# Performance work log

Measured on AMD Instinct MI355X. Metric: run time of the kernel, lower is better.

Reference implementation:

```python
import jax, jax.numpy as jnp
import numpy as np

N = 50000      # total nodes
E = 800000     # directed edges
G = 512        # graphs in batch
F_IN = 64      # node feature dim
H = 128        # hidden dim
L = 3          # gnn layers
OUT = 12       # tox21 tasks
EPS = 1e-5


def layer_norm(h, gamma, beta):
    mu = jnp.mean(h, axis=-1, keepdims=True)
    var = jnp.mean(jnp.square(h - mu), axis=-1, keepdims=True)
    return (h - mu) * jax.lax.rsqrt(var + EPS) * gamma + beta


def setup_inputs() -> dict:
    key = jax.random.key(0)
    ks = jax.random.split(key, 20)
    x = jax.random.normal(ks[0], (N, F_IN), jnp.float32)
    edge_index = jax.random.randint(ks[1], (2, E), 0, N, dtype=jnp.int64)
    batch_ids = jnp.sort(jax.random.randint(ks[2], (N,), 0, G, dtype=jnp.int64))
    s_in = 1.0 / np.sqrt(F_IN)
    s_h = 1.0 / np.sqrt(H)
    return {
        "x": x,
        "edge_index": edge_index,
        "batch_ids": batch_ids,
        "W_embed": jax.random.normal(ks[3], (F_IN, H), jnp.float32) * s_in,
        "b_embed": jnp.zeros((H,), jnp.float32),
        "g_embed": jnp.ones((H,), jnp.float32),
        "be_embed": jnp.zeros((H,), jnp.float32),
        "W_conv": jax.random.normal(ks[4], (L, H, H), jnp.float32) * s_h,
        "b_conv": jnp.zeros((L, H), jnp.float32),
        "g_ln": jnp.ones((L, H), jnp.float32),
        "b_ln": jnp.zeros((L, H), jnp.float32),
        "W_r1": jax.random.normal(ks[5], (H, H // 2), jnp.float32) * s_h,
        "b_r1": jnp.zeros((H // 2,), jnp.float32),
        "W_r2": jax.random.normal(ks[6], (H // 2, OUT), jnp.float32) * (1.0 / np.sqrt(H // 2)),
        "b_r2": jnp.zeros((OUT,), jnp.float32),
    }


def reference(x, edge_index, batch_ids, W_embed, b_embed, g_embed, be_embed,
              W_conv, b_conv, g_ln, b_ln, W_r1, b_r1, W_r2, b_r2):
    n = x.shape[0]
    # node embedding: Linear -> LayerNorm -> ReLU (dropout = eval identity)
    h = jax.nn.relu(layer_norm(x @ W_embed + b_embed, g_embed, be_embed))

    # GCN normalization with self-loops (PyG GCNConv semantics)
    loop = jnp.arange(n, dtype=edge_index.dtype)
    src = jnp.concatenate([edge_index[0], loop])  # message sources
    dst = jnp.concatenate([edge_index[1], loop])  # message targets
    deg = jax.ops.segment_sum(jnp.ones_like(dst, dtype=h.dtype), dst, num_segments=N)
    dinv = jnp.where(deg > 0, jax.lax.rsqrt(deg), 0.0)
    norm = dinv[src] * dinv[dst]  # [E+N]

    for i in range(L):
        h_prev = h
        m = h @ W_conv[i]                                        # [N,H] linear first
        msg = m[src] * norm[:, None]                             # gather + scale
        agg = jax.ops.segment_sum(msg, dst, num_segments=N)      # scatter-add
        agg = agg + b_conv[i]                                    # bias after aggregation
        h = jax.nn.relu(layer_norm(agg, g_ln[i], b_ln[i])) + h_prev  # norm+relu+residual

    # global mean pooling per graph
    counts = jax.ops.segment_sum(jnp.ones((n,), h.dtype), batch_ids, num_segments=G)
    pooled = jax.ops.segment_sum(h, batch_ids, num_segments=G) / jnp.maximum(counts, 1.0)[:, None]

    # readout MLP
    r = jax.nn.relu(pooled @ W_r1 + b_r1)
    return r @ W_r2 + b_r2
```

## Files before the change

### kernel.cpp

```cpp
#include <hip/hip_runtime.h>

#define HDIM 128
#define FIN 64
#define EPS 1e-5f
#define ECH 2048

typedef unsigned int uint;
typedef unsigned short ushort;
typedef __attribute__((ext_vector_type(8))) short bf16x8;
typedef __attribute__((ext_vector_type(4))) float f32x4;

__device__ __forceinline__ ushort f2bf(float f) {
    uint u = __float_as_uint(f);
    return (ushort)((u + 0x7fffu + ((u >> 16) & 1u)) >> 16);
}
__device__ __forceinline__ float bflo(uint u) { return __uint_as_float(u << 16); }
__device__ __forceinline__ float bfhi(uint u) { return __uint_as_float(u & 0xffff0000u); }

__global__ __launch_bounds__(256) void embed_fused(
    const float* __restrict__ x, const float* __restrict__ W,
    const float* __restrict__ b, const float* __restrict__ g,
    const float* __restrict__ be, ushort* __restrict__ hbf, int nrows,
    const int* __restrict__ dst, int* __restrict__ cnt, int e, int divc,
    const float* __restrict__ Wc, ushort* __restrict__ Wt)
{
    int t = threadIdx.x;
    int gtid = blockIdx.x * 256 + t;
    if (gtid < 3 * HDIM * HDIM) {
        int l = gtid >> 14, rem = gtid & 16383;
        int k = rem >> 7, nn = rem & 127;
        Wt[(l << 14) + nn * HDIM + k] = f2bf(Wc[gtid]);
    }
    int gpart = blockIdx.x & 7;
    int base = (blockIdx.x >> 3) * ECH;
    for (int i = t; i < ECH; i += 256) {
        int idx = base + i;
        if (idx < e) {
            int d = dst[idx];
            if ((int)((uint)d / (uint)divc) == gpart) atomicAdd(&cnt[d], 1);
        }
    }

    int row0 = blockIdx.x * 32;
    if (row0 >= nrows) return;

    __shared__ float Ws[FIN * HDIM];
    __shared__ float xs[32 * FIN];
    const float4* W4 = (const float4*)W;
    float4* Ws4 = (float4*)Ws;
#pragma unroll
    for (int i = 0; i < (FIN * HDIM / 4) / 256; i++) Ws4[t + i * 256] = W4[t + i * 256];
    int nr = nrows - row0; if (nr > 32) nr = 32;
    const float4* x4 = (const float4*)(x + (size_t)row0 * FIN);
    float4* xs4 = (float4*)xs;
    for (int i = t; i < nr * (FIN / 4); i += 256) xs4[i] = x4[i];
    __syncthreads();

    int c = (t & 31) * 4;
    int r0 = (t >> 5) * 4;
    float acc[4][4];
    float4 bv = *(const float4*)(b + c);
#pragma unroll
    for (int i = 0; i < 4; i++) { acc[i][0] = bv.x; acc[i][1] = bv.y; acc[i][2] = bv.z; acc[i][3] = bv.w; }
#pragma unroll 8
    for (int k = 0; k < FIN; k++) {
        float4 wv = *(const float4*)(Ws + k * HDIM + c);
#pragma unroll
        for (int i = 0; i < 4; i++) {
            float xv = xs[(r0 + i) * FIN + k];
            acc[i][0] += xv * wv.x; acc[i][1] += xv * wv.y;
            acc[i][2] += xv * wv.z; acc[i][3] += xv * wv.w;
        }
    }
    float4 gv = *(const float4*)(g + c);
    float4 bev = *(const float4*)(be + c);
#pragma unroll
    for (int i = 0; i < 4; i++) {
        float s1 = acc[i][0] + acc[i][1] + acc[i][2] + acc[i][3];
        float s2 = acc[i][0]*acc[i][0] + acc[i][1]*acc[i][1] + acc[i][2]*acc[i][2] + acc[i][3]*acc[i][3];
#pragma unroll
        for (int m = 16; m; m >>= 1) { s1 += __shfl_xor(s1, m); s2 += __shfl_xor(s2, m); }
        float mu = s1 * (1.0f / HDIM);
        float var = s2 * (1.0f / HDIM) - mu * mu;
        float rstd = rsqrtf(var + EPS);
        int row = row0 + r0 + i;
        if (row < nrows) {
            float ox = fmaxf((acc[i][0] - mu) * rstd * gv.x + bev.x, 0.f);
            float oy = fmaxf((acc[i][1] - mu) * rstd * gv.y + bev.y, 0.f);
            float oz = fmaxf((acc[i][2] - mu) * rstd * gv.z + bev.z, 0.f);
            float ow = fmaxf((acc[i][3] - mu) * rstd * gv.w + bev.w, 0.f);
            uint2 hb;
            hb.x = ((uint)f2bf(oy) << 16) | f2bf(ox);
            hb.y = ((uint)f2bf(ow) << 16) | f2bf(oz);
            *(uint2*)(hbf + (size_t)row * HDIM + c) = hb;
        }
    }
}

__global__ __launch_bounds__(256) void scan_sums(const int* __restrict__ cnt, int* __restrict__ bsum)
{
    __shared__ int s[256];
    int t = threadIdx.x;
    s[t] = cnt[blockIdx.x * 256 + t];
    __syncthreads();
    for (int d = 128; d; d >>= 1) { if (t < d) s[t] += s[t + d]; __syncthreads(); }
    if (t == 0) bsum[blockIdx.x] = s[0];
}

__global__ __launch_bounds__(256) void scan_final(
    const int* __restrict__ cnt, const int* __restrict__ bsum,
    int* __restrict__ rowstart, float* __restrict__ dinv, int nb)
{
    __shared__ int sb[256];
    __shared__ int s[256];
    int t = threadIdx.x;
    int vb = (t < nb) ? bsum[t] : 0;
    sb[t] = vb; __syncthreads();
    for (int d = 1; d < 256; d <<= 1) {
        int xv = (t >= d) ? sb[t - d] : 0;
        __syncthreads();
        sb[t] += xv;
        __syncthreads();
    }
    int blkoff = (blockIdx.x > 0) ? sb[blockIdx.x - 1] : 0;
    int gi = blockIdx.x * 256 + t;
    int c = cnt[gi];
    s[t] = c; __syncthreads();
    for (int d = 1; d < 256; d <<= 1) {
        int xv = (t >= d) ? s[t - d] : 0;
        __syncthreads();
        s[t] += xv;
        __syncthreads();
    }
    rowstart[gi] = blkoff + s[t] - c;
    dinv[gi] = rsqrtf((float)(c + 1));
}

__global__ __launch_bounds__(256) void fill_part(
    const int* __restrict__ src, const int* __restrict__ dst,
    const int* __restrict__ rowstart, int* __restrict__ fill,
    ushort* __restrict__ csr, int e, int divc)
{
    int g = blockIdx.x & 7;
    int base = (blockIdx.x >> 3) * ECH;
    for (int i = threadIdx.x; i < ECH; i += 256) {
        int idx = base + i;
        if (idx < e) {
            int d = dst[idx];
            if ((int)((uint)d / (uint)divc) == g) {
                int s = src[idx];
                int p = rowstart[d] + atomicAdd(&fill[d], 1);
                csr[p] = (ushort)s;
            }
        }
    }
}

__global__ __launch_bounds__(256) void gemm_mfma_kernel(
    const ushort* __restrict__ hbf, const ushort* __restrict__ Wt,
    const float* __restrict__ dinv, ushort* __restrict__ mbf, int nrows)
{
    __shared__ ushort hs[64 * HDIM];
    __shared__ ushort ws[HDIM * HDIM];
    int t = threadIdx.x;
    int wid = t >> 6, lane = t & 63;
    int row0 = blockIdx.x * 64;

#pragma unroll
    for (int it = 0; it < 4; it++) {
        int chunk = t * 4 + it;
        int r = chunk >> 4;
        int offb = (chunk & 15) * 16;
        int gr = row0 + r; if (gr >= nrows) gr = nrows - 1;
        uint4 d = *(const uint4*)(hbf + (size_t)gr * HDIM + (offb >> 1));
        *(uint4*)((char*)hs + r * 256 + (offb ^ ((r & 7) << 4))) = d;
    }
#pragma unroll
    for (int it = 0; it < 8; it++) {
        int chunk = t * 8 + it;
        int r = chunk >> 4;
        int offb = (chunk & 15) * 16;
        uint4 d = *(const uint4*)(Wt + (size_t)r * HDIM + (offb >> 1));
        *(uint4*)((char*)ws + r * 256 + (offb ^ ((r & 7) << 4))) = d;
    }
    __syncthreads();

    f32x4 acc[8];
#pragma unroll
    for (int nt = 0; nt < 8; nt++) acc[nt] = (f32x4){0.f, 0.f, 0.f, 0.f};

    int arow = wid * 16 + (lane & 15);
    int kgrp = (lane >> 4) * 16;
#pragma unroll
    for (int ks = 0; ks < 4; ks++) {
        int kb = ks * 64 + kgrp;
        bf16x8 afrag = *(const bf16x8*)((const char*)hs + arow * 256 + (kb ^ ((arow & 7) << 4)));
#pragma unroll
        for (int nt = 0; nt < 8; nt++) {
            int nrow = nt * 16 + (lane & 15);
            bf16x8 bfrag = *(const bf16x8*)((const char*)ws + nrow * 256 + (kb ^ ((nrow & 7) << 4)));
            acc[nt] = __builtin_amdgcn_mfma_f32_16x16x32_bf16(afrag, bfrag, acc[nt], 0, 0, 0);
        }
    }

    int rbase = row0 + wid * 16 + ((lane >> 4) << 2);
#pragma unroll
    for (int q = 0; q < 4; q++) {
        int grow = rbase + q;
        if (grow < nrows) {
            float dv = dinv[grow];
            ushort* orow = mbf + (size_t)grow * HDIM + (lane & 15);
#pragma unroll
            for (int nt = 0; nt < 8; nt++)
                orow[nt * 16] = f2bf(acc[nt][q] * dv);
        }
    }
}

__global__ __launch_bounds__(256) void agg_kernel(
    const ushort* __restrict__ mbf, const ushort* __restrict__ csr, const int* __restrict__ rowstart,
    const float* __restrict__ dinv, const float* __restrict__ bc,
    const float* __restrict__ gl, const float* __restrict__ bl,
    const ushort* __restrict__ hbf_in, ushort* __restrict__ hbf_out, int n)
{
    int wave = threadIdx.x >> 6, lane = threadIdx.x & 63;
    int v = blockIdx.x * 4 + wave;
    if (v >= n) return;
    const uint* m1 = (const uint*)mbf;
    uint aa = m1[(size_t)v * 64 + lane];
    float ax = bflo(aa), ay = bfhi(aa);
    int s0 = rowstart[v];
    int deg = rowstart[v + 1] - s0;
    for (int base = 0; base < deg; base += 64) {
        int idx = base + lane;
        int my = (idx < deg) ? (int)csr[s0 + idx] : 0;
        int cc = deg - base; if (cc > 64) cc = 64;
        int i = 0;
        for (; i + 4 <= cc; i += 4) {
            int u0 = __shfl(my, i);
            int u1 = __shfl(my, i + 1);
            int u2 = __shfl(my, i + 2);
            int u3 = __shfl(my, i + 3);
            uint w0 = m1[(size_t)u0 * 64 + lane];
            uint w1 = m1[(size_t)u1 * 64 + lane];
            uint w2 = m1[(size_t)u2 * 64 + lane];
            uint w3 = m1[(size_t)u3 * 64 + lane];
            ax += bflo(w0); ay += bfhi(w0);
            ax += bflo(w1); ay += bfhi(w1);
            ax += bflo(w2); ay += bfhi(w2);
            ax += bflo(w3); ay += bfhi(w3);
        }
        for (; i < cc; ++i) {
            int u0 = __shfl(my, i);
            uint w0 = m1[(size_t)u0 * 64 + lane];
            ax += bflo(w0); ay += bfhi(w0);
        }
    }
    float dvv = dinv[v];
    float2 bcv = ((const float2*)bc)[lane];
    float vx = ax * dvv + bcv.x;
    float vy = ay * dvv + bcv.y;
    float s1v = vx + vy, s2v = vx * vx + vy * vy;
#pragma unroll
    for (int m = 32; m; m >>= 1) { s1v += __shfl_xor(s1v, m); s2v += __shfl_xor(s2v, m); }
    float mu = s1v * (1.f / 128.f);
    float var = s2v * (1.f / 128.f) - mu * mu;
    float rstd = rsqrtf(var + EPS);
    float2 gv = ((const float2*)gl)[lane];
    float2 blv = ((const float2*)bl)[lane];
    uint hp = ((const uint*)hbf_in)[(size_t)v * 64 + lane];
    float ox = fmaxf((vx - mu) * rstd * gv.x + blv.x, 0.f) + bflo(hp);
    float oy = fmaxf((vy - mu) * rstd * gv.y + blv.y, 0.f) + bfhi(hp);
    ((uint*)hbf_out)[(size_t)v * 64 + lane] = ((uint)f2bf(oy) << 16) | f2bf(ox);
}

__global__ __launch_bounds__(256) void pool_readout(
    const ushort* __restrict__ hbf, const int* __restrict__ batch,
    const float* __restrict__ W1, const float* __restrict__ b1,
    const float* __restrict__ W2, const float* __restrict__ b2,
    float* __restrict__ out, int n, int G)
{
    int g = blockIdx.x, t = threadIdx.x;
    int lo = 0, hi = n;
    while (lo < hi) { int mid = (lo + hi) >> 1; if (batch[mid] < g) lo = mid + 1; else hi = mid; }
    int lo2 = lo, hi2 = n;
    while (lo2 < hi2) { int mid = (lo2 + hi2) >> 1; if (batch[mid] < g + 1) lo2 = mid + 1; else hi2 = mid; }
    int cp = t & 63, portion = t >> 6;
    float accx = 0.f, accy = 0.f;
    const uint* h1 = (const uint*)hbf;
    for (int nd = lo + portion; nd < lo2; nd += 4) {
        uint u = h1[(size_t)nd * 64 + cp];
        accx += bflo(u); accy += bfhi(u);
    }
    float cntf = (float)(lo2 - lo); if (cntf < 1.f) cntf = 1.f;
    __shared__ float psx[256], psy[256];
    __shared__ float ps[HDIM];
    __shared__ float rs[64];
    psx[t] = accx; psy[t] = accy;
    __syncthreads();
    if (t < 64) {
        float px = psx[t] + psx[t + 64] + psx[t + 128] + psx[t + 192];
        float py = psy[t] + psy[t + 64] + psy[t + 128] + psy[t + 192];
        ps[2 * t]     = px / cntf;
        ps[2 * t + 1] = py / cntf;
    }
    __syncthreads();
    if (t < 64) {
        float a = b1[t];
#pragma unroll 4
        for (int k = 0; k < HDIM; k++) a += ps[k] * W1[k * 64 + t];
        rs[t] = fmaxf(a, 0.f);
    }
    __syncthreads();
    if (t < 12) {
        float a = b2[t];
#pragma unroll
        for (int k = 0; k < 64; k++) a += rs[k] * W2[k * 12 + t];
        out[(size_t)g * 12 + t] = a;
    }
}

extern "C" void kernel_launch(void* const* d_in, const int* in_sizes, int n_in,
                              void* d_out, int out_size, void* d_ws, size_t ws_size,
                              hipStream_t stream) {
    const float* x       = (const float*)d_in[0];
    const int*   ei      = (const int*)d_in[1];
    const int*   batch   = (const int*)d_in[2];
    const float* W_embed = (const float*)d_in[3];
    const float* b_embed = (const float*)d_in[4];
    const float* g_embed = (const float*)d_in[5];
    const float* be_emb  = (const float*)d_in[6];
    const float* W_conv  = (const float*)d_in[7];
    const float* b_conv  = (const float*)d_in[8];
    const float* g_ln    = (const float*)d_in[9];
    const float* b_ln    = (const float*)d_in[10];
    const float* W_r1    = (const float*)d_in[11];
    const float* b_r1    = (const float*)d_in[12];
    const float* W_r2    = (const float*)d_in[13];
    const float* b_r2    = (const float*)d_in[14];
    float* out = (float*)d_out;

    int N = in_sizes[2];
    int E = in_sizes[1] / 2;
    int G = out_size / 12;
    int divc = (N + 7) / 8;
    int npad = ((N + 255) / 256) * 256;
    int NB = npad / 256;

    char* w = (char*)d_ws;
    ushort* hbf0 = (ushort*)w;  w += (size_t)N * HDIM * 2;
    ushort* hbf1 = (ushort*)w;  w += (size_t)N * HDIM * 2;
    ushort* mbf  = (ushort*)w;  w += (size_t)N * HDIM * 2;
    ushort* Wt   = (ushort*)w;  w += (size_t)3 * HDIM * HDIM * 2;
    float* dinv  = (float*)w;   w += (size_t)npad * 4;
    int* cnt     = (int*)w;     w += (size_t)npad * 4;
    int* fill    = (int*)w;     w += (size_t)npad * 4;
    int* rowstart= (int*)w;     w += (size_t)(npad + 4) * 4;
    int* bsum    = (int*)w;     w += 1024;
    ushort* csr  = (ushort*)w;  w += (size_t)E * 2;

    int nchunks = (E + ECH - 1) / ECH;
    int gridEC = nchunks * 8;

    hipMemsetAsync(cnt, 0, (size_t)2 * npad * 4, stream);

    embed_fused<<<gridEC, 256, 0, stream>>>(
        x, W_embed, b_embed, g_embed, be_emb, hbf0, N,
        ei + E, cnt, E, divc, W_conv, Wt);
    scan_sums<<<NB, 256, 0, stream>>>(cnt, bsum);
    scan_final<<<NB, 256, 0, stream>>>(cnt, bsum, rowstart, dinv, NB);
    fill_part<<<gridEC, 256, 0, stream>>>(ei, ei + E, rowstart, fill, csr, E, divc);

    const ushort* hin = hbf0;
    ushort* hout = hbf1;
    for (int l = 0; l < 3; l++) {
        gemm_mfma_kernel<<<(N + 63) / 64, 256, 0, stream>>>(
            hin, Wt + (size_t)l * HDIM * HDIM, dinv, mbf, N);
        agg_kernel<<<(N + 3) / 4, 256, 0, stream>>>(
            mbf, csr, rowstart, dinv, b_conv + l * HDIM, g_ln + l * HDIM, b_ln + l * HDIM,
            hin, hout, N);
        ushort* tmp = (ushort*)hin; hin = hout; hout = tmp;
    }
    pool_readout<<<G, 256, 0, stream>>>(hin, batch, W_r1, b_r1, W_r2, b_r2, out, N, G);
}
```

Before: 268.7 us.

## Split degree counting from embed, fold memset into embed, unroll aggregation gather by 8

Degree counting moves out of the embed kernel into its own count_part launch, and embed now launches only the row blocks it needs. The separate memset is replaced by zeroing the counters inside the embed kernel. The aggregation loop is unrolled to eight outstanding neighbor gathers, with a two-wide tail, and the residual load is hoisted to the top so memory latency overlaps. This adds one kernel launch and more registers in agg_kernel in exchange for more memory-level parallelism and less memset overhead.

```diff
diff --git a/kernel.cpp b/kernel.cpp
--- a/kernel.cpp
+++ b/kernel.cpp
@@ -17,32 +17,21 @@
 __device__ __forceinline__ float bflo(uint u) { return __uint_as_float(u << 16); }
 __device__ __forceinline__ float bfhi(uint u) { return __uint_as_float(u & 0xffff0000u); }
 
-__global__ __launch_bounds__(256) void embed_fused(
+__global__ __launch_bounds__(256) void embed_kernel(
     const float* __restrict__ x, const float* __restrict__ W,
     const float* __restrict__ b, const float* __restrict__ g,
     const float* __restrict__ be, ushort* __restrict__ hbf, int nrows,
-    const int* __restrict__ dst, int* __restrict__ cnt, int e, int divc,
+    int* __restrict__ zero_base, int zero_int4s,
     const float* __restrict__ Wc, ushort* __restrict__ Wt)
 {
     int t = threadIdx.x;
     int gtid = blockIdx.x * 256 + t;
+    if (gtid < zero_int4s) *(int4*)(zero_base + gtid * 4) = (int4){0, 0, 0, 0};
     if (gtid < 3 * HDIM * HDIM) {
         int l = gtid >> 14, rem = gtid & 16383;
         int k = rem >> 7, nn = rem & 127;
         Wt[(l << 14) + nn * HDIM + k] = f2bf(Wc[gtid]);
     }
-    int gpart = blockIdx.x & 7;
-    int base = (blockIdx.x >> 3) * ECH;
-    for (int i = t; i < ECH; i += 256) {
-        int idx = base + i;
-        if (idx < e) {
-            int d = dst[idx];
-            if ((int)((uint)d / (uint)divc) == gpart) atomicAdd(&cnt[d], 1);
-        }
-    }
-
-    int row0 = blockIdx.x * 32;
-    if (row0 >= nrows) return;
 
     __shared__ float Ws[FIN * HDIM];
     __shared__ float xs[32 * FIN];
@@ -50,6 +39,7 @@
     float4* Ws4 = (float4*)Ws;
 #pragma unroll
     for (int i = 0; i < (FIN * HDIM / 4) / 256; i++) Ws4[t + i * 256] = W4[t + i * 256];
+    int row0 = blockIdx.x * 32;
     int nr = nrows - row0; if (nr > 32) nr = 32;
     const float4* x4 = (const float4*)(x + (size_t)row0 * FIN);
     float4* xs4 = (float4*)xs;
@@ -97,6 +87,20 @@
     }
 }
 
+__global__ __launch_bounds__(256) void count_part(
+    const int* __restrict__ dst, int* __restrict__ cnt, int e, int divc)
+{
+    int g = blockIdx.x & 7;
+    int base = (blockIdx.x >> 3) * ECH;
+    for (int i = threadIdx.x; i < ECH; i += 256) {
+        int idx = base + i;
+        if (idx < e) {
+            int d = dst[idx];
+            if ((int)((uint)d / (uint)divc) == g) atomicAdd(&cnt[d], 1);
+        }
+    }
+}
+
 __global__ __launch_bounds__(256) void scan_sums(const int* __restrict__ cnt, int* __restrict__ bsum)
 {
     __shared__ int s[256];
@@ -227,6 +231,7 @@
     int v = blockIdx.x * 4 + wave;
     if (v >= n) return;
     const uint* m1 = (const uint*)mbf;
+    uint hp = ((const uint*)hbf_in)[(size_t)v * 64 + lane];
     uint aa = m1[(size_t)v * 64 + lane];
     float ax = bflo(aa), ay = bfhi(aa);
     int s0 = rowstart[v];
@@ -236,19 +241,39 @@
         int my = (idx < deg) ? (int)csr[s0 + idx] : 0;
         int cc = deg - base; if (cc > 64) cc = 64;
         int i = 0;
-        for (; i + 4 <= cc; i += 4) {
+        for (; i + 8 <= cc; i += 8) {
             int u0 = __shfl(my, i);
             int u1 = __shfl(my, i + 1);
             int u2 = __shfl(my, i + 2);
             int u3 = __shfl(my, i + 3);
+            int u4 = __shfl(my, i + 4);
+            int u5 = __shfl(my, i + 5);
+            int u6 = __shfl(my, i + 6);
+            int u7 = __shfl(my, i + 7);
             uint w0 = m1[(size_t)u0 * 64 + lane];
             uint w1 = m1[(size_t)u1 * 64 + lane];
             uint w2 = m1[(size_t)u2 * 64 + lane];
             uint w3 = m1[(size_t)u3 * 64 + lane];
+            uint w4 = m1[(size_t)u4 * 64 + lane];
+            uint w5 = m1[(size_t)u5 * 64 + lane];
+            uint w6 = m1[(size_t)u6 * 64 + lane];
+            uint w7 = m1[(size_t)u7 * 64 + lane];
             ax += bflo(w0); ay += bfhi(w0);
             ax += bflo(w1); ay += bfhi(w1);
             ax += bflo(w2); ay += bfhi(w2);
             ax += bflo(w3); ay += bfhi(w3);
+            ax += bflo(w4); ay += bfhi(w4);
+            ax += bflo(w5); ay += bfhi(w5);
+            ax += bflo(w6); ay += bfhi(w6);
+            ax += bflo(w7); ay += bfhi(w7);
+        }
+        for (; i + 2 <= cc; i += 2) {
+            int u0 = __shfl(my, i);
+            int u1 = __shfl(my, i + 1);
+            uint w0 = m1[(size_t)u0 * 64 + lane];
+            uint w1 = m1[(size_t)u1 * 64 + lane];
+            ax += bflo(w0); ay += bfhi(w0);
+            ax += bflo(w1); ay += bfhi(w1);
         }
         for (; i < cc; ++i) {
             int u0 = __shfl(my, i);
@@ -268,7 +293,6 @@
     float rstd = rsqrtf(var + EPS);
     float2 gv = ((const float2*)gl)[lane];
     float2 blv = ((const float2*)bl)[lane];
-    uint hp = ((const uint*)hbf_in)[(size_t)v * 64 + lane];
     float ox = fmaxf((vx - mu) * rstd * gv.x + blv.x, 0.f) + bflo(hp);
     float oy = fmaxf((vy - mu) * rstd * gv.y + blv.y, 0.f) + bfhi(hp);
     ((uint*)hbf_out)[(size_t)v * 64 + lane] = ((uint)f2bf(oy) << 16) | f2bf(ox);
@@ -361,12 +385,12 @@
 
     int nchunks = (E + ECH - 1) / ECH;
     int gridEC = nchunks * 8;
-
-    hipMemsetAsync(cnt, 0, (size_t)2 * npad * 4, stream);
-
-    embed_fused<<<gridEC, 256, 0, stream>>>(
+    int zero_int4s = (2 * npad) / 4;
+
+    embed_kernel<<<(N + 31) / 32, 256, 0, stream>>>(
         x, W_embed, b_embed, g_embed, be_emb, hbf0, N,
-        ei + E, cnt, E, divc, W_conv, Wt);
+        cnt, zero_int4s, W_conv, Wt);
+    count_part<<<gridEC, 256, 0, stream>>>(ei + E, cnt, E, divc);
     scan_sums<<<NB, 256, 0, stream>>>(cnt, bsum);
     scan_final<<<NB, 256, 0, stream>>>(cnt, bsum, rowstart, dinv, NB);
     fill_part<<<gridEC, 256, 0, stream>>>(ei, ei + E, rowstart, fill, csr, E, divc);
```

After: 274.6 us. 1.02x slower.

## Split edge counting from embed, drop memset, load GEMM operands directly from global

Applied to the files above, without the earlier changes.

Moves destination-degree counting out of the embed kernel into a separate count_part kernel. The hipMemsetAsync is replaced by having embed zero the count/fill arrays, and embed now launches one block per 32 rows. The per-layer GEMM no longer stages h and W through shared memory; each wave reads its A and B fragments straight from global memory, relying on cache for reuse of W. The agg kernel also issues the residual load earlier so it overlaps the gathers. This removes a memset and LDS staging and syncs, at the cost of an extra launch and repeated global reads of W.

```diff
diff --git a/kernel.cpp b/kernel.cpp
--- a/kernel.cpp
+++ b/kernel.cpp
@@ -17,32 +17,21 @@
 __device__ __forceinline__ float bflo(uint u) { return __uint_as_float(u << 16); }
 __device__ __forceinline__ float bfhi(uint u) { return __uint_as_float(u & 0xffff0000u); }
 
-__global__ __launch_bounds__(256) void embed_fused(
+__global__ __launch_bounds__(256) void embed_kernel(
     const float* __restrict__ x, const float* __restrict__ W,
     const float* __restrict__ b, const float* __restrict__ g,
     const float* __restrict__ be, ushort* __restrict__ hbf, int nrows,
-    const int* __restrict__ dst, int* __restrict__ cnt, int e, int divc,
+    int* __restrict__ zero_base, int zero_int4s,
     const float* __restrict__ Wc, ushort* __restrict__ Wt)
 {
     int t = threadIdx.x;
     int gtid = blockIdx.x * 256 + t;
+    if (gtid < zero_int4s) *(int4*)(zero_base + gtid * 4) = (int4){0, 0, 0, 0};
     if (gtid < 3 * HDIM * HDIM) {
         int l = gtid >> 14, rem = gtid & 16383;
         int k = rem >> 7, nn = rem & 127;
         Wt[(l << 14) + nn * HDIM + k] = f2bf(Wc[gtid]);
     }
-    int gpart = blockIdx.x & 7;
-    int base = (blockIdx.x >> 3) * ECH;
-    for (int i = t; i < ECH; i += 256) {
-        int idx = base + i;
-        if (idx < e) {
-            int d = dst[idx];
-            if ((int)((uint)d / (uint)divc) == gpart) atomicAdd(&cnt[d], 1);
-        }
-    }
-
-    int row0 = blockIdx.x * 32;
-    if (row0 >= nrows) return;
 
     __shared__ float Ws[FIN * HDIM];
     __shared__ float xs[32 * FIN];
@@ -50,6 +39,7 @@
     float4* Ws4 = (float4*)Ws;
 #pragma unroll
     for (int i = 0; i < (FIN * HDIM / 4) / 256; i++) Ws4[t + i * 256] = W4[t + i * 256];
+    int row0 = blockIdx.x * 32;
     int nr = nrows - row0; if (nr > 32) nr = 32;
     const float4* x4 = (const float4*)(x + (size_t)row0 * FIN);
     float4* xs4 = (float4*)xs;
@@ -97,6 +87,20 @@
     }
 }
 
+__global__ __launch_bounds__(256) void count_part(
+    const int* __restrict__ dst, int* __restrict__ cnt, int e, int divc)
+{
+    int g = blockIdx.x & 7;
+    int base = (blockIdx.x >> 3) * ECH;
+    for (int i = threadIdx.x; i < ECH; i += 256) {
+        int idx = base + i;
+        if (idx < e) {
+            int d = dst[idx];
+            if ((int)((uint)d / (uint)divc) == g) atomicAdd(&cnt[d], 1);
+        }
+    }
+}
+
 __global__ __launch_bounds__(256) void scan_sums(const int* __restrict__ cnt, int* __restrict__ bsum)
 {
     __shared__ int s[256];
@@ -160,46 +164,28 @@
     const ushort* __restrict__ hbf, const ushort* __restrict__ Wt,
     const float* __restrict__ dinv, ushort* __restrict__ mbf, int nrows)
 {
-    __shared__ ushort hs[64 * HDIM];
-    __shared__ ushort ws[HDIM * HDIM];
     int t = threadIdx.x;
     int wid = t >> 6, lane = t & 63;
     int row0 = blockIdx.x * 64;
-
-#pragma unroll
-    for (int it = 0; it < 4; it++) {
-        int chunk = t * 4 + it;
-        int r = chunk >> 4;
-        int offb = (chunk & 15) * 16;
-        int gr = row0 + r; if (gr >= nrows) gr = nrows - 1;
-        uint4 d = *(const uint4*)(hbf + (size_t)gr * HDIM + (offb >> 1));
-        *(uint4*)((char*)hs + r * 256 + (offb ^ ((r & 7) << 4))) = d;
-    }
-#pragma unroll
-    for (int it = 0; it < 8; it++) {
-        int chunk = t * 8 + it;
-        int r = chunk >> 4;
-        int offb = (chunk & 15) * 16;
-        uint4 d = *(const uint4*)(Wt + (size_t)r * HDIM + (offb >> 1));
-        *(uint4*)((char*)ws + r * 256 + (offb ^ ((r & 7) << 4))) = d;
-    }
-    __syncthreads();
+    int arow = row0 + wid * 16 + (lane & 15);
+    int arcl = (arow < nrows) ? arow : (nrows - 1);
+    int kgrp = lane >> 4;
+    const ushort* aptr = hbf + (size_t)arcl * HDIM + kgrp * 8;
+
+    bf16x8 af[4];
+#pragma unroll
+    for (int ks = 0; ks < 4; ks++)
+        af[ks] = *(const bf16x8*)(aptr + ks * 32);
 
     f32x4 acc[8];
 #pragma unroll
-    for (int nt = 0; nt < 8; nt++) acc[nt] = (f32x4){0.f, 0.f, 0.f, 0.f};
-
-    int arow = wid * 16 + (lane & 15);
-    int kgrp = (lane >> 4) * 16;
-#pragma unroll
-    for (int ks = 0; ks < 4; ks++) {
-        int kb = ks * 64 + kgrp;
-        bf16x8 afrag = *(const bf16x8*)((const char*)hs + arow * 256 + (kb ^ ((arow & 7) << 4)));
-#pragma unroll
-        for (int nt = 0; nt < 8; nt++) {
-            int nrow = nt * 16 + (lane & 15);
-            bf16x8 bfrag = *(const bf16x8*)((const char*)ws + nrow * 256 + (kb ^ ((nrow & 7) << 4)));
-            acc[nt] = __builtin_amdgcn_mfma_f32_16x16x32_bf16(afrag, bfrag, acc[nt], 0, 0, 0);
+    for (int nt = 0; nt < 8; nt++) {
+        acc[nt] = (f32x4){0.f, 0.f, 0.f, 0.f};
+        const ushort* bp = Wt + (size_t)(nt * 16 + (lane & 15)) * HDIM + kgrp * 8;
+#pragma unroll
+        for (int ks = 0; ks < 4; ks++) {
+            bf16x8 bfrag = *(const bf16x8*)(bp + ks * 32);
+            acc[nt] = __builtin_amdgcn_mfma_f32_16x16x32_bf16(af[ks], bfrag, acc[nt], 0, 0, 0);
         }
     }
 
@@ -227,6 +213,7 @@
     int v = blockIdx.x * 4 + wave;
     if (v >= n) return;
     const uint* m1 = (const uint*)mbf;
+    uint hp = ((const uint*)hbf_in)[(size_t)v * 64 + lane];
     uint aa = m1[(size_t)v * 64 + lane];
     float ax = bflo(aa), ay = bfhi(aa);
     int s0 = rowstart[v];
@@ -268,7 +255,6 @@
     float rstd = rsqrtf(var + EPS);
     float2 gv = ((const float2*)gl)[lane];
     float2 blv = ((const float2*)bl)[lane];
-    uint hp = ((const uint*)hbf_in)[(size_t)v * 64 + lane];
     float ox = fmaxf((vx - mu) * rstd * gv.x + blv.x, 0.f) + bflo(hp);
     float oy = fmaxf((vy - mu) * rstd * gv.y + blv.y, 0.f) + bfhi(hp);
     ((uint*)hbf_out)[(size_t)v * 64 + lane] = ((uint)f2bf(oy) << 16) | f2bf(ox);
@@ -361,12 +347,12 @@
 
     int nchunks = (E + ECH - 1) / ECH;
     int gridEC = nchunks * 8;
-
-    hipMemsetAsync(cnt, 0, (size_t)2 * npad * 4, stream);
-
-    embed_fused<<<gridEC, 256, 0, stream>>>(
+    int zero_int4s = (2 * npad) / 4;
+
+    embed_kernel<<<(N + 31) / 32, 256, 0, stream>>>(
         x, W_embed, b_embed, g_embed, be_emb, hbf0, N,
-        ei + E, cnt, E, divc, W_conv, Wt);
+        cnt, zero_int4s, W_conv, Wt);
+    count_part<<<gridEC, 256, 0, stream>>>(ei + E, cnt, E, divc);
     scan_sums<<<NB, 256, 0, stream>>>(cnt, bsum);
     scan_final<<<NB, 256, 0, stream>>>(cnt, bsum, rowstart, dinv, NB);
     fill_part<<<gridEC, 256, 0, stream>>>(ei, ei + E, rowstart, fill, csr, E, divc);
```

Result: slower. 306.5 us (+14.1%).
